# Kernel tuning notes

Measured on AMD Instinct MI355X. Metric: run time of the kernel, lower is better.

Reference implementation:

```python
import jax, jax.numpy as jnp
import numpy as np

NUM_HEADS = 16
B, S, H = 2, 8192, 1024


def setup_inputs() -> dict:
    key = jax.random.key(0)
    ks = jax.random.split(key, 6)
    scale = 1.0 / np.sqrt(H)
    return {
        "hidden_states": jax.random.normal(ks[0], (B, S, H), dtype=jnp.float32),
        "Wq": jax.random.normal(ks[1], (H, H), dtype=jnp.float32) * scale,
        "Wk": jax.random.normal(ks[2], (H, H), dtype=jnp.float32) * scale,
        "Wv": jax.random.normal(ks[3], (H, H), dtype=jnp.float32) * scale,
        "Wg": jax.random.normal(ks[4], (H, H), dtype=jnp.float32) * scale,
        "Wo": jax.random.normal(ks[5], (H, H), dtype=jnp.float32) * scale,
        "gamma": jnp.ones((H,), dtype=jnp.float32),
        "beta": jnp.zeros((H,), dtype=jnp.float32),
    }


def reference(hidden_states, Wq, Wk, Wv, Wg, Wo, gamma, beta):
    b, s, h = hidden_states.shape
    nh = NUM_HEADS
    dk = h // nh
    dv = h // nh
    # projections (bias-free linears)
    q = (hidden_states @ Wq).reshape(b, s, nh, dk)
    k = (hidden_states @ Wk).reshape(b, s, nh, dk)
    v = (hidden_states @ Wv).reshape(b, s, nh, dv)
    g = hidden_states @ Wg  # [b, s, h]
    # elu+1 feature map
    q = jax.nn.elu(q) + 1.0
    k = jax.nn.elu(k) + 1.0
    # kv = k outer v per token, then contracted with q  ==> (q.k) * v (no [b,h,n,d,e] tensor)
    qk = jnp.sum(q * k, axis=-1, keepdims=True)        # [b, s, nh, 1]
    k_sum = jnp.sum(k, axis=1, keepdims=True)          # [b, 1, nh, dk] (global over seq)
    normalizer = jnp.sum(q * k_sum, axis=-1, keepdims=True)  # [b, s, nh, 1]
    z = qk * v / (normalizer + 1e-6)                   # [b, s, nh, dv]
    z = z.reshape(b, s, nh * dv)
    # LayerNorm (eps=1e-5, affine)
    mu = jnp.mean(z, axis=-1, keepdims=True)
    var = jnp.mean(jnp.square(z - mu), axis=-1, keepdims=True)
    z = (z - mu) * jax.lax.rsqrt(var + 1e-5) * gamma + beta
    # SiLU gating and output projection
    z = z * jax.nn.silu(g)
    return z @ Wo
```

## Files before the change

kernel.cpp:

```cpp
#include <hip/hip_runtime.h>


typedef unsigned short ushort_t;
typedef unsigned int uint_t;

using short8  = __attribute__((ext_vector_type(8))) short;
using floatx4 = __attribute__((ext_vector_type(4))) float;

#define HDIM  1024
#define T_TOK 16384
#define KSPLIT 3072

__device__ __forceinline__ ushort_t f2bf(float f) {
    uint_t u = __builtin_bit_cast(uint_t, f);
    u = (u + 0x7fff + ((u >> 16) & 1)) >> 16;
    return (ushort_t)u;
}
__device__ __forceinline__ float bf2f(ushort_t h) {
    uint_t u = ((uint_t)h) << 16;
    return __builtin_bit_cast(float, u);
}
__device__ __forceinline__ void split2(float f, ushort_t& hi, ushort_t& lo) {
    hi = f2bf(f);
    lo = f2bf(f - bf2f(hi));
}
__device__ __forceinline__ void gload_lds16(const ushort_t* g, ushort_t* l) {
    __builtin_amdgcn_global_load_lds(
        (const __attribute__((address_space(1))) void*)g,
        (__attribute__((address_space(3))) void*)l, 16, 0, 0);
}

__global__ void split_w(const float* __restrict__ W0, const float* __restrict__ W1,
                        const float* __restrict__ W2, const float* __restrict__ W3,
                        const float* __restrict__ W4, ushort_t* __restrict__ WT2) {
    __shared__ float tile[32][33];
    const int z = blockIdx.z;
    const float* W = (z == 0) ? W0 : (z == 1) ? W1 : (z == 2) ? W2 : (z == 3) ? W3 : W4;
    ushort_t* dst = WT2 + (size_t)z * HDIM * 2048;
    const int n0 = blockIdx.x * 32, k0 = blockIdx.y * 32;
    const int tx = threadIdx.x & 31, ty0 = threadIdx.x >> 5;
#pragma unroll
    for (int s = 0; s < 4; ++s) {
        int ty = ty0 + 8 * s;
        tile[ty][tx] = W[(size_t)(k0 + ty) * HDIM + n0 + tx];
    }
    __syncthreads();
#pragma unroll
    for (int s = 0; s < 4; ++s) {
        int ty = ty0 + 8 * s;
        float v = tile[tx][ty];
        ushort_t hi, lo;
        split2(v, hi, lo);
        dst[(size_t)(n0 + ty) * 2048 + k0 + tx] = hi;
        dst[(size_t)(n0 + ty) * 2048 + 1024 + k0 + tx] = lo;
    }
}

__global__ __launch_bounds__(256)
void split_hidden(const float* __restrict__ h, ushort_t* __restrict__ Hs) {
    const int t = blockIdx.x;
    const int c = threadIdx.x;
    const float4 x = ((const float4*)(h + (size_t)t * HDIM))[c];
    ushort_t hi[4], lo[4];
    split2(x.x, hi[0], lo[0]); split2(x.y, hi[1], lo[1]);
    split2(x.z, hi[2], lo[2]); split2(x.w, hi[3], lo[3]);
    ushort_t* row = Hs + (size_t)t * 2048;
    uint2 hp, lp;
    hp.x = (uint_t)hi[0] | ((uint_t)hi[1] << 16);
    hp.y = (uint_t)hi[2] | ((uint_t)hi[3] << 16);
    lp.x = (uint_t)lo[0] | ((uint_t)lo[1] << 16);
    lp.y = (uint_t)lo[2] | ((uint_t)lo[3] << 16);
    *(uint2*)(row + c * 4) = hp;
    *(uint2*)(row + 1024 + c * 4) = lp;
}

template <int EPI>
__global__ __launch_bounds__(256)
void gemm_swz(const ushort_t* __restrict__ A, const ushort_t* __restrict__ Bw,
              float* __restrict__ D, const float* __restrict__ kf,
              const float* __restrict__ ksum, float* __restrict__ scbuf,
              ushort_t* __restrict__ zbuf) {
    __shared__ ushort_t As[128 * 64];
    __shared__ ushort_t Bs[128 * 64];
    const int tid = threadIdx.x;
    const int bx = blockIdx.x, by = blockIdx.y;
    const int w = tid >> 6, lane = tid & 63;
    const int wm = w & 1, wn = w >> 1;
    const int lrow = lane & 15, lq = lane >> 4;

    const int srow = lane >> 3;
    const int scol = ((lane & 7) ^ srow) * 8;
    const ushort_t* Ag = A + (size_t)(bx * 128 + w * 32 + srow) * 2048 + scol;
    const ushort_t* Bg = Bw + (size_t)(by * 128 + w * 32 + srow) * 2048 + scol;

    floatx4 acc[4][4] = {};

    for (int k0 = 0; k0 < KSPLIT; k0 += 64) {
        const int ka = k0 - ((k0 >= 2048) ? 2048 : 0);
        const int kb = k0 - ((k0 >= 1024) ? 1024 : 0);
        __syncthreads();
#pragma unroll
        for (int n = 0; n < 4; ++n) {
            gload_lds16(Ag + (size_t)(n * 8) * 2048 + ka, &As[(w * 32 + n * 8) * 64]);
            gload_lds16(Bg + (size_t)(n * 8) * 2048 + kb, &Bs[(w * 32 + n * 8) * 64]);
        }
        __syncthreads();
#pragma unroll
        for (int kk = 0; kk < 64; kk += 32) {
            short8 af[4], bf[4];
#pragma unroll
            for (int i = 0; i < 4; ++i) {
                const int c = (((kk >> 3) + lq) ^ (lrow & 7)) * 8;
                af[i] = *(const short8*)&As[(wm * 64 + i * 16 + lrow) * 64 + c];
            }
#pragma unroll
            for (int j = 0; j < 4; ++j) {
                const int c = (((kk >> 3) + lq) ^ (lrow & 7)) * 8;
                bf[j] = *(const short8*)&Bs[(wn * 64 + j * 16 + lrow) * 64 + c];
            }
#pragma unroll
            for (int i = 0; i < 4; ++i)
#pragma unroll
                for (int j = 0; j < 4; ++j)
                    acc[i][j] = __builtin_amdgcn_mfma_f32_16x16x32_bf16(af[i], bf[j], acc[i][j], 0, 0, 0);
        }
    }

    const int rowbase = bx * 128 + wm * 64 + lq * 4;
    const int colbase = by * 128 + wn * 64 + lrow;

    if (EPI == 0 || EPI == 2) {
#pragma unroll
        for (int i = 0; i < 4; ++i)
#pragma unroll
            for (int j = 0; j < 4; ++j) {
                const int col = colbase + j * 16;
#pragma unroll
                for (int r = 0; r < 4; ++r) {
                    const int row = rowbase + i * 16 + r;
                    float val = acc[i][j][r];
                    if (EPI == 0) val = (val > 0.0f) ? (val + 1.0f) : (expm1f(val) + 1.0f);
                    D[(size_t)row * HDIM + col] = val;
                }
            }
    } else if (EPI == 1) {
        const int b = (bx * 128) >> 13;
        float ksv[4];
#pragma unroll
        for (int j = 0; j < 4; ++j) ksv[j] = ksum[b * HDIM + colbase + j * 16];
        const int h = by * 2 + wn;
#pragma unroll
        for (int i = 0; i < 4; ++i)
#pragma unroll
            for (int r = 0; r < 4; ++r) {
                const int row = rowbase + i * 16 + r;
                float qk = 0.f, nm = 0.f;
#pragma unroll
                for (int j = 0; j < 4; ++j) {
                    float qv = acc[i][j][r];
                    qv = (qv > 0.0f) ? (qv + 1.0f) : (expm1f(qv) + 1.0f);
                    const float kv = kf[(size_t)row * HDIM + colbase + j * 16];
                    qk += qv * kv;
                    nm += qv * ksv[j];
                }
#pragma unroll
                for (int off = 1; off < 16; off <<= 1) {
                    qk += __shfl_xor(qk, off, 64);
                    nm += __shfl_xor(nm, off, 64);
                }
                if (lrow == 0) scbuf[row * 16 + h] = qk / (nm + 1e-6f);
            }
    } else {
#pragma unroll
        for (int i = 0; i < 4; ++i)
#pragma unroll
            for (int j = 0; j < 4; ++j) {
                const int col = colbase + j * 16;
#pragma unroll
                for (int r = 0; r < 4; ++r) {
                    const int row = rowbase + i * 16 + r;
                    ushort_t* zr = zbuf + (size_t)row * 2048;
                    const float zn = bf2f(zr[col]) + bf2f(zr[1024 + col]);
                    const float g = acc[i][j][r];
                    const float sg = g / (1.0f + expf(-g));
                    ushort_t hi, lo;
                    split2(zn * sg, hi, lo);
                    zr[col] = hi;
                    zr[1024 + col] = lo;
                }
            }
    }
}

__global__ void ksum_partial(const float* __restrict__ kf, float* __restrict__ partial) {
    const int rg = blockIdx.x;
    const int tid = threadIdx.x;
    const float4* p = (const float4*)(kf + (size_t)rg * 64 * HDIM) + tid;
    float4 s = {0.f, 0.f, 0.f, 0.f};
    for (int r = 0; r < 64; ++r) {
        float4 x = p[(size_t)r * (HDIM / 4)];
        s.x += x.x; s.y += x.y; s.z += x.z; s.w += x.w;
    }
    ((float4*)(partial + (size_t)rg * HDIM))[tid] = s;
}
__global__ void ksum_reduce(const float* __restrict__ partial, float* __restrict__ ksum) {
    const int b = blockIdx.y;
    const int c = blockIdx.x * 256 + threadIdx.x;
    float s = 0.f;
    const float* p = partial + (size_t)b * 128 * HDIM + c;
    for (int rg = 0; rg < 128; ++rg) s += p[(size_t)rg * HDIM];
    ksum[b * HDIM + c] = s;
}

__global__ __launch_bounds__(256)
void token_lite(float* vz, const float* __restrict__ scbuf) {
    const int t = blockIdx.x;
    const int tid = threadIdx.x;
    const float4 v = ((const float4*)(vz + (size_t)t * HDIM))[tid];
    const float sc = scbuf[t * 16 + (tid >> 4)];
    float z[4] = {v.x * sc, v.y * sc, v.z * sc, v.w * sc};

    __shared__ float red[8];
    const int wv = tid >> 6, lane = tid & 63;

    float s1 = z[0] + z[1] + z[2] + z[3];
#pragma unroll
    for (int off = 1; off < 64; off <<= 1) s1 += __shfl_xor(s1, off, 64);
    if (lane == 0) red[wv] = s1;
    __syncthreads();
    const float mu = (red[0] + red[1] + red[2] + red[3]) * (1.0f / 1024.0f);

    float d[4] = {z[0] - mu, z[1] - mu, z[2] - mu, z[3] - mu};
    float s2 = d[0] * d[0] + d[1] * d[1] + d[2] * d[2] + d[3] * d[3];
#pragma unroll
    for (int off = 1; off < 64; off <<= 1) s2 += __shfl_xor(s2, off, 64);
    __syncthreads();
    if (lane == 0) red[4 + wv] = s2;
    __syncthreads();
    const float var = (red[4] + red[5] + red[6] + red[7]) * (1.0f / 1024.0f);
    const float rstd = rsqrtf(var + 1e-5f);

    ushort_t* zrow = (ushort_t*)(vz + (size_t)t * HDIM);
    ushort_t hi[4], lo[4];
#pragma unroll
    for (int c = 0; c < 4; ++c) split2(d[c] * rstd, hi[c], lo[c]);
    uint2 hp, lp;
    hp.x = (uint_t)hi[0] | ((uint_t)hi[1] << 16);
    hp.y = (uint_t)hi[2] | ((uint_t)hi[3] << 16);
    lp.x = (uint_t)lo[0] | ((uint_t)lo[1] << 16);
    lp.y = (uint_t)lo[2] | ((uint_t)lo[3] << 16);
    *(uint2*)(zrow + tid * 4) = hp;
    *(uint2*)(zrow + 1024 + tid * 4) = lp;
}

template <int DUMMY>
__global__ __launch_bounds__(256)
void gemm_gate(const ushort_t* __restrict__ A, const ushort_t* __restrict__ Bw,
               const float* __restrict__ gamma, const float* __restrict__ beta,
               ushort_t* __restrict__ zbuf) {
    __shared__ ushort_t As[128 * 64];
    __shared__ ushort_t Bs[128 * 64];
    const int tid = threadIdx.x;
    const int bx = blockIdx.x, by = blockIdx.y;
    const int w = tid >> 6, lane = tid & 63;
    const int wm = w & 1, wn = w >> 1;
    const int lrow = lane & 15, lq = lane >> 4;

    const int srow = lane >> 3;
    const int scol = ((lane & 7) ^ srow) * 8;
    const ushort_t* Ag = A + (size_t)(bx * 128 + w * 32 + srow) * 2048 + scol;
    const ushort_t* Bg = Bw + (size_t)(by * 128 + w * 32 + srow) * 2048 + scol;

    floatx4 acc[4][4] = {};

    for (int k0 = 0; k0 < KSPLIT; k0 += 64) {
        const int ka = k0 - ((k0 >= 2048) ? 2048 : 0);
        const int kb = k0 - ((k0 >= 1024) ? 1024 : 0);
        __syncthreads();
#pragma unroll
        for (int n = 0; n < 4; ++n) {
            gload_lds16(Ag + (size_t)(n * 8) * 2048 + ka, &As[(w * 32 + n * 8) * 64]);
            gload_lds16(Bg + (size_t)(n * 8) * 2048 + kb, &Bs[(w * 32 + n * 8) * 64]);
        }
        __syncthreads();
#pragma unroll
        for (int kk = 0; kk < 64; kk += 32) {
            short8 af[4], bf[4];
#pragma unroll
            for (int i = 0; i < 4; ++i) {
                const int c = (((kk >> 3) + lq) ^ (lrow & 7)) * 8;
                af[i] = *(const short8*)&As[(wm * 64 + i * 16 + lrow) * 64 + c];
            }
#pragma unroll
            for (int j = 0; j < 4; ++j) {
                const int c = (((kk >> 3) + lq) ^ (lrow & 7)) * 8;
                bf[j] = *(const short8*)&Bs[(wn * 64 + j * 16 + lrow) * 64 + c];
            }
#pragma unroll
            for (int i = 0; i < 4; ++i)
#pragma unroll
                for (int j = 0; j < 4; ++j)
                    acc[i][j] = __builtin_amdgcn_mfma_f32_16x16x32_bf16(af[i], bf[j], acc[i][j], 0, 0, 0);
        }
    }

    const int rowbase = bx * 128 + wm * 64 + lq * 4;
    const int colbase = by * 128 + wn * 64 + lrow;
#pragma unroll
    for (int i = 0; i < 4; ++i)
#pragma unroll
        for (int j = 0; j < 4; ++j) {
            const int col = colbase + j * 16;
            const float gam = gamma[col], bet = beta[col];
#pragma unroll
            for (int r = 0; r < 4; ++r) {
                const int row = rowbase + i * 16 + r;
                ushort_t* zr = zbuf + (size_t)row * 2048;
                const float zn = bf2f(zr[col]) + bf2f(zr[1024 + col]);
                const float g = acc[i][j][r];
                const float sg = g / (1.0f + expf(-g));
                ushort_t hi, lo;
                split2((zn * gam + bet) * sg, hi, lo);
                zr[col] = hi;
                zr[1024 + col] = lo;
            }
        }
}

template <int VAR>
__global__ __launch_bounds__(256, 2)
void gemm_split(const float* __restrict__ A,
                const ushort_t* __restrict__ B0, const ushort_t* __restrict__ B1,
                const ushort_t* __restrict__ B2,
                float* __restrict__ D0, float* __restrict__ D1, float* __restrict__ D2,
                int K) {
    __shared__ ushort_t Ah[128 * 72];
    __shared__ ushort_t Al[128 * 72];
    __shared__ ushort_t Bh[128 * 72];
    __shared__ ushort_t Bl[128 * 72];
    const int tid = threadIdx.x;
    const int bx = blockIdx.x, by = blockIdx.y;
    const ushort_t* Bt;
    float* D;
    int n0;
    bool act;
    if (VAR == 1) {
        const int wsel = by >> 3;
        Bt = (wsel == 0) ? B0 : (wsel == 1) ? B1 : B2;
        D = (wsel == 0) ? D0 : (wsel == 1) ? D1 : D2;
        n0 = (by & 7) * 128;
        act = (wsel == 0);
    } else {
        Bt = B0; D = D0; n0 = by * 128; act = true;
    }
    const int w = tid >> 6, lane = tid & 63;
    const int wm = w & 1, wn = w >> 1;
    const int lrow = lane & 15, lq = lane >> 4;
    const int srow = tid >> 1;
    const int shalf = (tid & 1) * 32;
    const float* Arow = A + (size_t)(bx * 128 + srow) * K;
    const ushort_t* Brow = Bt + (size_t)(n0 + srow) * 2048;
    floatx4 acc[4][4] = {};
    for (int k0 = 0; k0 < K; k0 += 64) {
        float4 afr[8];
        uint4 bhr[4], blr[4];
#pragma unroll
        for (int g = 0; g < 4; ++g) {
            afr[2 * g]     = *(const float4*)(Arow + k0 + shalf + g * 8);
            afr[2 * g + 1] = *(const float4*)(Arow + k0 + shalf + g * 8 + 4);
            bhr[g] = *(const uint4*)(Brow + k0 + shalf + g * 8);
            blr[g] = *(const uint4*)(Brow + 1024 + k0 + shalf + g * 8);
        }
        __syncthreads();
#pragma unroll
        for (int g = 0; g < 4; ++g) {
            ushort_t h[8], l[8];
            const float4 f0 = afr[2 * g], f1 = afr[2 * g + 1];
            split2(f0.x, h[0], l[0]); split2(f0.y, h[1], l[1]);
            split2(f0.z, h[2], l[2]); split2(f0.w, h[3], l[3]);
            split2(f1.x, h[4], l[4]); split2(f1.y, h[5], l[5]);
            split2(f1.z, h[6], l[6]); split2(f1.w, h[7], l[7]);
            uint4 hp, lp;
            hp.x = (uint_t)h[0] | ((uint_t)h[1] << 16);
            hp.y = (uint_t)h[2] | ((uint_t)h[3] << 16);
            hp.z = (uint_t)h[4] | ((uint_t)h[5] << 16);
            hp.w = (uint_t)h[6] | ((uint_t)h[7] << 16);
            lp.x = (uint_t)l[0] | ((uint_t)l[1] << 16);
            lp.y = (uint_t)l[2] | ((uint_t)l[3] << 16);
            lp.z = (uint_t)l[4] | ((uint_t)l[5] << 16);
            lp.w = (uint_t)l[6] | ((uint_t)l[7] << 16);
            *(uint4*)&Ah[srow * 72 + shalf + g * 8] = hp;
            *(uint4*)&Al[srow * 72 + shalf + g * 8] = lp;
            *(uint4*)&Bh[srow * 72 + shalf + g * 8] = bhr[g];
            *(uint4*)&Bl[srow * 72 + shalf + g * 8] = blr[g];
        }
        __syncthreads();
#pragma unroll
        for (int kk = 0; kk < 64; kk += 32) {
            short8 ah[4], bh[4], xl[4];
#pragma unroll
            for (int i = 0; i < 4; ++i)
                ah[i] = *(const short8*)&Ah[(wm * 64 + i * 16 + lrow) * 72 + kk + lq * 8];
#pragma unroll
            for (int j = 0; j < 4; ++j)
                bh[j] = *(const short8*)&Bh[(wn * 64 + j * 16 + lrow) * 72 + kk + lq * 8];
#pragma unroll
            for (int i = 0; i < 4; ++i)
#pragma unroll
                for (int j = 0; j < 4; ++j)
                    acc[i][j] = __builtin_amdgcn_mfma_f32_16x16x32_bf16(ah[i], bh[j], acc[i][j], 0, 0, 0);
#pragma unroll
            for (int i = 0; i < 4; ++i)
                xl[i] = *(const short8*)&Al[(wm * 64 + i * 16 + lrow) * 72 + kk + lq * 8];
#pragma unroll
            for (int i = 0; i < 4; ++i)
#pragma unroll
                for (int j = 0; j < 4; ++j)
                    acc[i][j] = __builtin_amdgcn_mfma_f32_16x16x32_bf16(xl[i], bh[j], acc[i][j], 0, 0, 0);
#pragma unroll
            for (int j = 0; j < 4; ++j)
                xl[j] = *(const short8*)&Bl[(wn * 64 + j * 16 + lrow) * 72 + kk + lq * 8];
#pragma unroll
            for (int i = 0; i < 4; ++i)
#pragma unroll
                for (int j = 0; j < 4; ++j)
                    acc[i][j] = __builtin_amdgcn_mfma_f32_16x16x32_bf16(ah[i], xl[j], acc[i][j], 0, 0, 0);
        }
    }
    const int rowbase = bx * 128 + wm * 64 + lq * 4;
    const int colbase = n0 + wn * 64 + lrow;
#pragma unroll
    for (int i = 0; i < 4; ++i)
#pragma unroll
        for (int j = 0; j < 4; ++j) {
            const int col = colbase + j * 16;
#pragma unroll
            for (int r = 0; r < 4; ++r) {
                const int row = rowbase + i * 16 + r;
                float val = acc[i][j][r];
                if (act) val = (val > 0.0f) ? (val + 1.0f) : (expm1f(val) + 1.0f);
                D[(size_t)row * HDIM + col] = val;
            }
        }
}

__global__ __launch_bounds__(256)
void token_f32(const float* __restrict__ qd, const float* __restrict__ vd,
               const float* __restrict__ gd, float* kz,
               const float* __restrict__ ksum,
               const float* __restrict__ gamma, const float* __restrict__ beta,
               int chunk_base) {
    const int tl = blockIdx.x;
    const int t = chunk_base + tl;
    const int b = t >> 13;
    const int tid = threadIdx.x;
    const float4 q = ((const float4*)(qd + (size_t)tl * HDIM))[tid];
    const float4 k = ((const float4*)(kz + (size_t)t * HDIM))[tid];
    const float4 v = ((const float4*)(vd + (size_t)tl * HDIM))[tid];
    const float4 ks = ((const float4*)(ksum + (size_t)b * HDIM))[tid];
    float qk = q.x * k.x + q.y * k.y + q.z * k.z + q.w * k.w;
    float nm = q.x * ks.x + q.y * ks.y + q.z * ks.z + q.w * ks.w;
#pragma unroll
    for (int off = 1; off < 16; off <<= 1) {
        qk += __shfl_xor(qk, off, 64);
        nm += __shfl_xor(nm, off, 64);
    }
    const float sc = qk / (nm + 1e-6f);
    float z[4] = {v.x * sc, v.y * sc, v.z * sc, v.w * sc};
    __shared__ float red[8];
    const int wv = tid >> 6, lane = tid & 63;
    float s1 = z[0] + z[1] + z[2] + z[3];
#pragma unroll
    for (int off = 1; off < 64; off <<= 1) s1 += __shfl_xor(s1, off, 64);
    if (lane == 0) red[wv] = s1;
    __syncthreads();
    const float mu = (red[0] + red[1] + red[2] + red[3]) * (1.0f / 1024.0f);
    float d[4] = {z[0] - mu, z[1] - mu, z[2] - mu, z[3] - mu};
    float s2 = d[0] * d[0] + d[1] * d[1] + d[2] * d[2] + d[3] * d[3];
#pragma unroll
    for (int off = 1; off < 64; off <<= 1) s2 += __shfl_xor(s2, off, 64);
    __syncthreads();
    if (lane == 0) red[4 + wv] = s2;
    __syncthreads();
    const float var = (red[4] + red[5] + red[6] + red[7]) * (1.0f / 1024.0f);
    const float rstd = rsqrtf(var + 1e-5f);
    const float4 gm = ((const float4*)gamma)[tid];
    const float4 bt = ((const float4*)beta)[tid];
    const float4 g = ((const float4*)(gd + (size_t)tl * HDIM))[tid];
    const float gv[4] = {g.x, g.y, g.z, g.w};
    const float gmv[4] = {gm.x, gm.y, gm.z, gm.w};
    const float btv[4] = {bt.x, bt.y, bt.z, bt.w};
    ushort_t hi[4], lo[4];
#pragma unroll
    for (int c = 0; c < 4; ++c) {
        const float zn = d[c] * rstd * gmv[c] + btv[c];
        const float sg = gv[c] / (1.0f + expf(-gv[c]));
        split2(zn * sg, hi[c], lo[c]);
    }
    ushort_t* zrow = (ushort_t*)(kz + (size_t)t * HDIM);
    uint2 hp, lp;
    hp.x = (uint_t)hi[0] | ((uint_t)hi[1] << 16);
    hp.y = (uint_t)hi[2] | ((uint_t)hi[3] << 16);
    lp.x = (uint_t)lo[0] | ((uint_t)lo[1] << 16);
    lp.y = (uint_t)lo[2] | ((uint_t)lo[3] << 16);
    *(uint2*)(zrow + tid * 4) = hp;
    *(uint2*)(zrow + 1024 + tid * 4) = lp;
}

extern "C" void kernel_launch(void* const* d_in, const int* in_sizes, int n_in,
                              void* d_out, int out_size, void* d_ws, size_t ws_size,
                              hipStream_t stream) {
    const float* hidden = (const float*)d_in[0];
    const float* Wq = (const float*)d_in[1];
    const float* Wk = (const float*)d_in[2];
    const float* Wv = (const float*)d_in[3];
    const float* Wg = (const float*)d_in[4];
    const float* Wo = (const float*)d_in[5];
    const float* gamma = (const float*)d_in[6];
    const float* beta = (const float*)d_in[7];

    char* w = (char*)d_ws;
    float* kb = (float*)w;            w += (size_t)67108864;
    ushort_t* WT2 = (ushort_t*)w;     w += (size_t)20971520;
    float* partial = (float*)w;       w += (size_t)1048576;
    float* ksum = (float*)w;          w += (size_t)8192;
    float* scbuf = (float*)w;         w += (size_t)1048576;
    const size_t base = (size_t)(w - (char*)d_ws);

    ushort_t* Wk2 = WT2;
    ushort_t* Wq2 = WT2 + (size_t)1 * HDIM * 2048;
    ushort_t* Wv2 = WT2 + (size_t)2 * HDIM * 2048;
    ushort_t* Wg2 = WT2 + (size_t)3 * HDIM * 2048;
    ushort_t* Wo2 = WT2 + (size_t)4 * HDIM * 2048;

    split_w<<<dim3(32, 32, 5), 256, 0, stream>>>(Wk, Wq, Wv, Wg, Wo, WT2);

    if (ws_size >= base + 67108864ull) {
        ushort_t* Hs = (ushort_t*)w;
        split_hidden<<<dim3(T_TOK), 256, 0, stream>>>(hidden, Hs);
        gemm_swz<0><<<dim3(128, 8), 256, 0, stream>>>(Hs, Wk2, kb, nullptr, nullptr,
                                                      nullptr, nullptr);
        ksum_partial<<<dim3(256), 256, 0, stream>>>(kb, partial);
        ksum_reduce<<<dim3(4, 2), 256, 0, stream>>>(partial, ksum);
        gemm_swz<1><<<dim3(128, 8), 256, 0, stream>>>(Hs, Wq2, nullptr, kb, ksum,
                                                      scbuf, nullptr);
        gemm_swz<2><<<dim3(128, 8), 256, 0, stream>>>(Hs, Wv2, kb, nullptr, nullptr,
                                                      nullptr, nullptr);
        token_lite<<<dim3(T_TOK), 256, 0, stream>>>(kb, scbuf);
        gemm_gate<0><<<dim3(128, 8), 256, 0, stream>>>(Hs, Wg2, gamma, beta,
                                                       (ushort_t*)kb);
        gemm_swz<2><<<dim3(128, 8), 256, 0, stream>>>((const ushort_t*)kb, Wo2,
                                                      (float*)d_out, nullptr, nullptr,
                                                      nullptr, nullptr);
    } else {
        const int C = 2048;
        float* qc = (float*)w;
        float* vc = qc + (size_t)C * HDIM;
        float* gc = vc + (size_t)C * HDIM;
        gemm_split<0><<<dim3(128, 8), 256, 0, stream>>>(hidden, Wk2, nullptr, nullptr,
                                                        kb, nullptr, nullptr, HDIM);
        ksum_partial<<<dim3(256), 256, 0, stream>>>(kb, partial);
        ksum_reduce<<<dim3(4, 2), 256, 0, stream>>>(partial, ksum);
        for (int c = 0; c < 8; ++c) {
            const float* Ac = hidden + (size_t)c * C * HDIM;
            gemm_split<1><<<dim3(C / 128, 24), 256, 0, stream>>>(Ac, Wq2, Wv2, Wg2,
                                                                 qc, vc, gc, HDIM);
            token_f32<<<dim3(C), 256, 0, stream>>>(qc, vc, gc, kb, ksum,
                                                   gamma, beta, c * C);
        }
        gemm_swz<2><<<dim3(128, 8), 256, 0, stream>>>((const ushort_t*)kb, Wo2,
                                                      (float*)d_out, nullptr, nullptr,
                                                      nullptr, nullptr);
    }
}
```

Before: 810.1 us.

## Replace 128x128 GEMMs with double-buffered 256x256 tile kernel with interleaved prefetch

Introduces a new gemm256 kernel with 512 threads, 256x256 output tiles, double-buffered LDS staging, and a hand-scheduled loop. The loop interleaves global-to-LDS loads for the next K step with MFMA phases and raises wave priority around the MFMA blocks. All five projection GEMMs in the main path, including the gated LayerNorm epilogue, now use this kernel. The goal is more reuse per tile and hiding load latency behind matrix math, at the cost of heavy register and LDS use (128KB LDS, 32 accumulator tiles per wave). The grid also shrinks to 256 blocks, which may leave some compute units underused.

```diff
diff --git a/kernel.cpp b/kernel.cpp
--- a/kernel.cpp
+++ b/kernel.cpp
@@ -74,6 +74,192 @@
     *(uint2*)(row + 1024 + c * 4) = lp;
 }
 
+
+#define FENCE() asm volatile("" ::: "memory")
+#define BAR1()  do { FENCE(); __builtin_amdgcn_s_barrier(); FENCE(); \
+                     __builtin_amdgcn_sched_barrier(0); } while (0)
+#define BAR2()  do { FENCE(); __builtin_amdgcn_s_barrier(); FENCE(); } while (0)
+#define VMW4()  asm volatile("s_waitcnt vmcnt(4)" ::: "memory")
+
+#define STG_A(t, h, bsel) do { \
+    const int ka_ = ((t) * 64 >= 2048) ? ((t) * 64 - 2048) : ((t) * 64); \
+    gload_lds16(Ag + (size_t)((h) * 128) * 2048 + ka_, \
+                &As[(bsel) * 16384 + ((h) * 128 + w * 16) * 64]); \
+    gload_lds16(Ag + (size_t)((h) * 128 + 8) * 2048 + ka_, \
+                &As[(bsel) * 16384 + ((h) * 128 + w * 16 + 8) * 64]); \
+  } while (0)
+
+#define STG_B(t, h, bsel) do { \
+    const int kb_ = ((t) * 64 >= 1024) ? ((t) * 64 - 1024) : ((t) * 64); \
+    gload_lds16(Bg + (size_t)((h) * 128) * 2048 + kb_, \
+                &Bs[(bsel) * 16384 + ((h) * 128 + w * 16) * 64]); \
+    gload_lds16(Bg + (size_t)((h) * 128 + 8) * 2048 + kb_, \
+                &Bs[(bsel) * 16384 + ((h) * 128 + w * 16 + 8) * 64]); \
+  } while (0)
+
+#define RD_AF(p, bsel) do { \
+    af[0][0] = *(const short8*)(Ar0 + (bsel) * 16384 + (2 * (p)) * 1024); \
+    af[0][1] = *(const short8*)(Ar1 + (bsel) * 16384 + (2 * (p)) * 1024); \
+    af[1][0] = *(const short8*)(Ar0 + (bsel) * 16384 + (2 * (p) + 1) * 1024); \
+    af[1][1] = *(const short8*)(Ar1 + (bsel) * 16384 + (2 * (p) + 1) * 1024); \
+  } while (0)
+
+#define RD_BF(bsel) do { \
+    _Pragma("unroll") \
+    for (int j = 0; j < 4; ++j) { \
+        bf[j][0] = *(const short8*)(Br0 + (bsel) * 16384 + j * 1024); \
+        bf[j][1] = *(const short8*)(Br1 + (bsel) * 16384 + j * 1024); \
+    } \
+  } while (0)
+
+#define MM(p) do { \
+    __builtin_amdgcn_s_setprio(1); \
+    _Pragma("unroll") \
+    for (int di = 0; di < 2; ++di) \
+    _Pragma("unroll") \
+    for (int j = 0; j < 4; ++j) { \
+        acc[2 * (p) + di][j] = __builtin_amdgcn_mfma_f32_16x16x32_bf16( \
+            af[di][0], bf[j][0], acc[2 * (p) + di][j], 0, 0, 0); \
+        acc[2 * (p) + di][j] = __builtin_amdgcn_mfma_f32_16x16x32_bf16( \
+            af[di][1], bf[j][1], acc[2 * (p) + di][j], 0, 0, 0); \
+    } \
+    __builtin_amdgcn_s_setprio(0); \
+  } while (0)
+
+template <int EPI>
+__global__ __launch_bounds__(512, 2)
+void gemm256(const ushort_t* __restrict__ A, const ushort_t* __restrict__ Bw,
+             float* __restrict__ D, const float* __restrict__ kf,
+             const float* __restrict__ ksum, float* __restrict__ scbuf,
+             ushort_t* __restrict__ zbuf, const float* __restrict__ gamma,
+             const float* __restrict__ beta) {
+    __shared__ ushort_t As[2 * 256 * 64];
+    __shared__ ushort_t Bs[2 * 256 * 64];
+    const int tid = threadIdx.x;
+    const int bx = blockIdx.x, by = blockIdx.y;
+    const int w = tid >> 6, lane = tid & 63;
+    const int wm = w & 1, wn = w >> 1;
+    const int lrow = lane & 15, lq = lane >> 4;
+
+    const int srow = lane >> 3;
+    const int scol = ((lane & 7) ^ srow) * 8;
+    const ushort_t* Ag = A + (size_t)(bx * 256 + w * 16 + srow) * 2048 + scol;
+    const ushort_t* Bg = Bw + (size_t)(by * 256 + w * 16 + srow) * 2048 + scol;
+
+    const int c0 = (lq ^ (lrow & 7)) * 8;
+    const int c1 = ((lq + 4) ^ (lrow & 7)) * 8;
+    const ushort_t* Ar0 = As + (wm * 128 + lrow) * 64 + c0;
+    const ushort_t* Ar1 = As + (wm * 128 + lrow) * 64 + c1;
+    const ushort_t* Br0 = Bs + (wn * 64 + lrow) * 64 + c0;
+    const ushort_t* Br1 = Bs + (wn * 64 + lrow) * 64 + c1;
+
+    floatx4 acc[8][4] = {};
+    short8 bf[4][2];
+    short8 af[2][2];
+
+    STG_A(0, 0, 0); STG_A(0, 1, 0);
+    STG_B(0, 0, 0); STG_B(0, 1, 0);
+    STG_B(1, 0, 1); STG_B(1, 1, 1);
+    VMW4();
+    BAR2();
+
+#pragma unroll 1
+    for (int t = 0; t < 48; t += 2) {
+        RD_BF(0); RD_AF(0, 0);
+        STG_A(t + 1, 0, 1); STG_A(t + 1, 1, 1);
+        BAR1(); MM(0); BAR2();
+        RD_AF(1, 0);
+        STG_B(t + 2, 0, 0);
+        BAR1(); MM(1); BAR2();
+        RD_AF(2, 0);
+        STG_B(t + 2, 1, 0);
+        BAR1(); MM(2); BAR2();
+        RD_AF(3, 0);
+        BAR1(); MM(3);
+        VMW4();
+        BAR2();
+        RD_BF(1); RD_AF(0, 1);
+        STG_A(t + 2, 0, 0); STG_A(t + 2, 1, 0);
+        BAR1(); MM(0); BAR2();
+        RD_AF(1, 1);
+        STG_B(t + 3, 0, 1);
+        BAR1(); MM(1); BAR2();
+        RD_AF(2, 1);
+        STG_B(t + 3, 1, 1);
+        BAR1(); MM(2); BAR2();
+        RD_AF(3, 1);
+        BAR1(); MM(3);
+        VMW4();
+        BAR2();
+    }
+
+    const int rowbase = bx * 256 + wm * 128 + lq * 4;
+    const int colbase = by * 256 + wn * 64 + lrow;
+
+    if constexpr (EPI == 0 || EPI == 2) {
+#pragma unroll
+        for (int i = 0; i < 8; ++i)
+#pragma unroll
+            for (int j = 0; j < 4; ++j) {
+                const int col = colbase + j * 16;
+#pragma unroll
+                for (int r = 0; r < 4; ++r) {
+                    const int row = rowbase + i * 16 + r;
+                    float val = acc[i][j][r];
+                    if (EPI == 0) val = (val > 0.0f) ? (val + 1.0f) : (expm1f(val) + 1.0f);
+                    D[(size_t)row * HDIM + col] = val;
+                }
+            }
+    } else if constexpr (EPI == 1) {
+        const int b = bx >> 5;
+        float ksv[4];
+#pragma unroll
+        for (int j = 0; j < 4; ++j) ksv[j] = ksum[b * HDIM + colbase + j * 16];
+        const int h = by * 4 + wn;
+#pragma unroll
+        for (int i = 0; i < 8; ++i)
+#pragma unroll
+            for (int r = 0; r < 4; ++r) {
+                const int row = rowbase + i * 16 + r;
+                float qk = 0.f, nm = 0.f;
+#pragma unroll
+                for (int j = 0; j < 4; ++j) {
+                    float qv = acc[i][j][r];
+                    qv = (qv > 0.0f) ? (qv + 1.0f) : (expm1f(qv) + 1.0f);
+                    const float kv = kf[(size_t)row * HDIM + colbase + j * 16];
+                    qk += qv * kv;
+                    nm += qv * ksv[j];
+                }
+#pragma unroll
+                for (int off = 1; off < 16; off <<= 1) {
+                    qk += __shfl_xor(qk, off, 64);
+                    nm += __shfl_xor(nm, off, 64);
+                }
+                if (lrow == 0) scbuf[row * 16 + h] = qk / (nm + 1e-6f);
+            }
+    } else {
+#pragma unroll
+        for (int i = 0; i < 8; ++i)
+#pragma unroll
+            for (int j = 0; j < 4; ++j) {
+                const int col = colbase + j * 16;
+                const float gam = gamma[col], bet = beta[col];
+#pragma unroll
+                for (int r = 0; r < 4; ++r) {
+                    const int row = rowbase + i * 16 + r;
+                    ushort_t* zr = zbuf + (size_t)row * 2048;
+                    const float zn = bf2f(zr[col]) + bf2f(zr[1024 + col]);
+                    const float g = acc[i][j][r];
+                    const float sg = g / (1.0f + expf(-g));
+                    ushort_t hi, lo;
+                    split2((zn * gam + bet) * sg, hi, lo);
+                    zr[col] = hi;
+                    zr[1024 + col] = lo;
+                }
+            }
+    }
+}
+
 template <int EPI>
 __global__ __launch_bounds__(256)
 void gemm_swz(const ushort_t* __restrict__ A, const ushort_t* __restrict__ Bw,
@@ -128,68 +314,19 @@
 
     const int rowbase = bx * 128 + wm * 64 + lq * 4;
     const int colbase = by * 128 + wn * 64 + lrow;
-
-    if (EPI == 0 || EPI == 2) {
-#pragma unroll
-        for (int i = 0; i < 4; ++i)
-#pragma unroll
-            for (int j = 0; j < 4; ++j) {
-                const int col = colbase + j * 16;
-#pragma unroll
-                for (int r = 0; r < 4; ++r) {
-                    const int row = rowbase + i * 16 + r;
-                    float val = acc[i][j][r];
-                    if (EPI == 0) val = (val > 0.0f) ? (val + 1.0f) : (expm1f(val) + 1.0f);
-                    D[(size_t)row * HDIM + col] = val;
-                }
-            }
-    } else if (EPI == 1) {
-        const int b = (bx * 128) >> 13;
-        float ksv[4];
-#pragma unroll
-        for (int j = 0; j < 4; ++j) ksv[j] = ksum[b * HDIM + colbase + j * 16];
-        const int h = by * 2 + wn;
-#pragma unroll
-        for (int i = 0; i < 4; ++i)
+#pragma unroll
+    for (int i = 0; i < 4; ++i)
+#pragma unroll
+        for (int j = 0; j < 4; ++j) {
+            const int col = colbase + j * 16;
 #pragma unroll
             for (int r = 0; r < 4; ++r) {
                 const int row = rowbase + i * 16 + r;
-                float qk = 0.f, nm = 0.f;
-#pragma unroll
-                for (int j = 0; j < 4; ++j) {
-                    float qv = acc[i][j][r];
-                    qv = (qv > 0.0f) ? (qv + 1.0f) : (expm1f(qv) + 1.0f);
-                    const float kv = kf[(size_t)row * HDIM + colbase + j * 16];
-                    qk += qv * kv;
-                    nm += qv * ksv[j];
-                }
-#pragma unroll
-                for (int off = 1; off < 16; off <<= 1) {
-                    qk += __shfl_xor(qk, off, 64);
-                    nm += __shfl_xor(nm, off, 64);
-                }
-                if (lrow == 0) scbuf[row * 16 + h] = qk / (nm + 1e-6f);
+                float val = acc[i][j][r];
+                if (EPI == 0) val = (val > 0.0f) ? (val + 1.0f) : (expm1f(val) + 1.0f);
+                D[(size_t)row * HDIM + col] = val;
             }
-    } else {
-#pragma unroll
-        for (int i = 0; i < 4; ++i)
-#pragma unroll
-            for (int j = 0; j < 4; ++j) {
-                const int col = colbase + j * 16;
-#pragma unroll
-                for (int r = 0; r < 4; ++r) {
-                    const int row = rowbase + i * 16 + r;
-                    ushort_t* zr = zbuf + (size_t)row * 2048;
-                    const float zn = bf2f(zr[col]) + bf2f(zr[1024 + col]);
-                    const float g = acc[i][j][r];
-                    const float sg = g / (1.0f + expf(-g));
-                    ushort_t hi, lo;
-                    split2(zn * sg, hi, lo);
-                    zr[col] = hi;
-                    zr[1024 + col] = lo;
-                }
-            }
-    }
+        }
 }
 
 __global__ void ksum_partial(const float* __restrict__ kf, float* __restrict__ partial) {
@@ -251,80 +388,6 @@
     lp.y = (uint_t)lo[2] | ((uint_t)lo[3] << 16);
     *(uint2*)(zrow + tid * 4) = hp;
     *(uint2*)(zrow + 1024 + tid * 4) = lp;
-}
-
-template <int DUMMY>
-__global__ __launch_bounds__(256)
-void gemm_gate(const ushort_t* __restrict__ A, const ushort_t* __restrict__ Bw,
-               const float* __restrict__ gamma, const float* __restrict__ beta,
-               ushort_t* __restrict__ zbuf) {
-    __shared__ ushort_t As[128 * 64];
-    __shared__ ushort_t Bs[128 * 64];
-    const int tid = threadIdx.x;
-    const int bx = blockIdx.x, by = blockIdx.y;
-    const int w = tid >> 6, lane = tid & 63;
-    const int wm = w & 1, wn = w >> 1;
-    const int lrow = lane & 15, lq = lane >> 4;
-
-    const int srow = lane >> 3;
-    const int scol = ((lane & 7) ^ srow) * 8;
-    const ushort_t* Ag = A + (size_t)(bx * 128 + w * 32 + srow) * 2048 + scol;
-    const ushort_t* Bg = Bw + (size_t)(by * 128 + w * 32 + srow) * 2048 + scol;
-
-    floatx4 acc[4][4] = {};
-
-    for (int k0 = 0; k0 < KSPLIT; k0 += 64) {
-        const int ka = k0 - ((k0 >= 2048) ? 2048 : 0);
-        const int kb = k0 - ((k0 >= 1024) ? 1024 : 0);
-        __syncthreads();
-#pragma unroll
-        for (int n = 0; n < 4; ++n) {
-            gload_lds16(Ag + (size_t)(n * 8) * 2048 + ka, &As[(w * 32 + n * 8) * 64]);
-            gload_lds16(Bg + (size_t)(n * 8) * 2048 + kb, &Bs[(w * 32 + n * 8) * 64]);
-        }
-        __syncthreads();
-#pragma unroll
-        for (int kk = 0; kk < 64; kk += 32) {
-            short8 af[4], bf[4];
-#pragma unroll
-            for (int i = 0; i < 4; ++i) {
-                const int c = (((kk >> 3) + lq) ^ (lrow & 7)) * 8;
-                af[i] = *(const short8*)&As[(wm * 64 + i * 16 + lrow) * 64 + c];
-            }
-#pragma unroll
-            for (int j = 0; j < 4; ++j) {
-                const int c = (((kk >> 3) + lq) ^ (lrow & 7)) * 8;
-                bf[j] = *(const short8*)&Bs[(wn * 64 + j * 16 + lrow) * 64 + c];
-            }
-#pragma unroll
-            for (int i = 0; i < 4; ++i)
-#pragma unroll
-                for (int j = 0; j < 4; ++j)
-                    acc[i][j] = __builtin_amdgcn_mfma_f32_16x16x32_bf16(af[i], bf[j], acc[i][j], 0, 0, 0);
-        }
-    }
-
-    const int rowbase = bx * 128 + wm * 64 + lq * 4;
-    const int colbase = by * 128 + wn * 64 + lrow;
-#pragma unroll
-    for (int i = 0; i < 4; ++i)
-#pragma unroll
-        for (int j = 0; j < 4; ++j) {
-            const int col = colbase + j * 16;
-            const float gam = gamma[col], bet = beta[col];
-#pragma unroll
-            for (int r = 0; r < 4; ++r) {
-                const int row = rowbase + i * 16 + r;
-                ushort_t* zr = zbuf + (size_t)row * 2048;
-                const float zn = bf2f(zr[col]) + bf2f(zr[1024 + col]);
-                const float g = acc[i][j][r];
-                const float sg = g / (1.0f + expf(-g));
-                ushort_t hi, lo;
-                split2((zn * gam + bet) * sg, hi, lo);
-                zr[col] = hi;
-                zr[1024 + col] = lo;
-            }
-        }
 }
 
 template <int VAR>
@@ -538,20 +601,20 @@
     if (ws_size >= base + 67108864ull) {
         ushort_t* Hs = (ushort_t*)w;
         split_hidden<<<dim3(T_TOK), 256, 0, stream>>>(hidden, Hs);
-        gemm_swz<0><<<dim3(128, 8), 256, 0, stream>>>(Hs, Wk2, kb, nullptr, nullptr,
-                                                      nullptr, nullptr);
+        gemm256<0><<<dim3(64, 4), 512, 0, stream>>>(Hs, Wk2, kb, nullptr, nullptr,
+                                                    nullptr, nullptr, nullptr, nullptr);
         ksum_partial<<<dim3(256), 256, 0, stream>>>(kb, partial);
         ksum_reduce<<<dim3(4, 2), 256, 0, stream>>>(partial, ksum);
-        gemm_swz<1><<<dim3(128, 8), 256, 0, stream>>>(Hs, Wq2, nullptr, kb, ksum,
-                                                      scbuf, nullptr);
-        gemm_swz<2><<<dim3(128, 8), 256, 0, stream>>>(Hs, Wv2, kb, nullptr, nullptr,
-                                                      nullptr, nullptr);
+        gemm256<1><<<dim3(64, 4), 512, 0, stream>>>(Hs, Wq2, nullptr, kb, ksum,
+                                                    scbuf, nullptr, nullptr, nullptr);
+        gemm256<2><<<dim3(64, 4), 512, 0, stream>>>(Hs, Wv2, kb, nullptr, nullptr,
+                                                    nullptr, nullptr, nullptr, nullptr);
         token_lite<<<dim3(T_TOK), 256, 0, stream>>>(kb, scbuf);
-        gemm_gate<0><<<dim3(128, 8), 256, 0, stream>>>(Hs, Wg2, gamma, beta,
-                                                       (ushort_t*)kb);
-        gemm_swz<2><<<dim3(128, 8), 256, 0, stream>>>((const ushort_t*)kb, Wo2,
-                                                      (float*)d_out, nullptr, nullptr,
-                                                      nullptr, nullptr);
+        gemm256<3><<<dim3(64, 4), 512, 0, stream>>>(Hs, Wg2, nullptr, nullptr, nullptr,
+                                                    nullptr, (ushort_t*)kb, gamma, beta);
+        gemm256<2><<<dim3(64, 4), 512, 0, stream>>>((const ushort_t*)kb, Wo2,
+                                                    (float*)d_out, nullptr, nullptr,
+                                                    nullptr, nullptr, nullptr, nullptr);
     } else {
         const int C = 2048;
         float* qc = (float*)w;
```

Measured after the change: 679.0 us. 16.2% less time.
